# Kernel tuning notes

Hardware: AMD Instinct MI355X
Metric: run time of the kernel (lower is better)

## Reference

```python
import jax, jax.numpy as jnp
import numpy as np

N = 10000
D1, D2, D3, N_INPUT = 20, 256, 128, 500


def setup_inputs() -> dict:
    key = jax.random.key(0)
    k1, k2, k3, k4, k5 = jax.random.split(key, 5)
    z_igae = jax.random.normal(k1, (N, D1), dtype=jnp.float32)
    # row-stochastic-ish dense (normalized) adjacency stand-in
    adj = jax.random.uniform(k2, (N, N), dtype=jnp.float32) / N
    w3 = jax.random.normal(k3, (D1, D2), dtype=jnp.float32) * 0.1
    w4 = jax.random.normal(k4, (D2, D3), dtype=jnp.float32) * 0.1
    w5 = jax.random.normal(k5, (D3, N_INPUT), dtype=jnp.float32) * 0.1
    return {"z_igae": z_igae, "adj": adj, "w3": w3, "w4": w4, "w5": w5}


def reference(z_igae, adj, w3, w4, w5):
    # GNNLayer: spmm(adj, x @ W), tanh activation when active=True
    z = jnp.tanh(adj @ (z_igae @ w3))        # [N, D2]
    z = jnp.tanh(adj @ (z @ w4))             # [N, D3]
    z_hat = adj @ (z @ w5)                   # [N, n_input], active=False
    z_hat_adj = jax.nn.sigmoid(z_hat @ z_hat.T)  # [N, N] dense reconstruction
    return (z_hat, z_hat_adj)
```

## Files before the change

kernel.cpp:

```cpp
#include <hip/hip_runtime.h>
#include <cstddef>
#include <cstdint>


typedef __attribute__((ext_vector_type(8))) short bf16x8;
typedef __attribute__((ext_vector_type(4))) float f32x4;

#define NROWS 10000
#define MP    10048
#define MPAD  10112

__device__ inline unsigned short f2bf(float f) {
  union { float f; unsigned int u; } a; a.f = f;
  unsigned int u = a.u;
  u += 0x7fffu + ((u >> 16) & 1u);
  return (unsigned short)(u >> 16);
}

__device__ inline void gl_lds16(const void* g, void* l) {
  __builtin_amdgcn_global_load_lds(
      (const __attribute__((address_space(1))) void*)g,
      (__attribute__((address_space(3))) void*)l, 16, 0, 0);
}

__global__ __launch_bounds__(256)
void gemm1_fused(const float* __restrict__ adj, const short* __restrict__ zt,
                 short* __restrict__ adjb, float* __restrict__ P,
                 int kChunks, int S) {
  __shared__ short As[64 * 64];
  __shared__ short Bs[32 * 64];
  const int tid  = threadIdx.x;
  const int wave = tid >> 6;
  const int lane = tid & 63;
  const int row0 = blockIdx.y * 64;
  const int s    = blockIdx.z;
  const int t0 = (int)((long long)s * kChunks / S);
  const int t1 = (int)((long long)(s + 1) * kChunks / S);

  f32x4 acc[2];
#pragma unroll
  for (int i = 0; i < 2; ++i) acc[i] = (f32x4){0.f, 0.f, 0.f, 0.f};

  const int lr = lane >> 3;
  const int lk = ((lane & 7) ^ lr) * 8;
  const int fr = lane & 15, fq = lane >> 4, sw = lane & 7;

  const int ar  = tid >> 2;
  const int acq = tid & 3;
  const int gr  = row0 + ar;
  const bool rv = gr < NROWS;

  for (int t = t0; t < t1; ++t) {
    const int k0 = t * 64;
    __syncthreads();
    gl_lds16(zt + (size_t)(8 * wave + lr) * MP + k0 + lk, (void*)(Bs + wave * 512));
    const int gc = k0 + acq * 16;
    float4 f[4];
#pragma unroll
    for (int j = 0; j < 4; ++j) {
      int c = gc + 4 * j;
      f[j] = (rv && c < NROWS) ? *(const float4*)(adj + (size_t)gr * NROWS + c)
                               : make_float4(0.f, 0.f, 0.f, 0.f);
    }
    unsigned short h[16] __attribute__((aligned(16)));
#pragma unroll
    for (int j = 0; j < 4; ++j) {
      h[4 * j + 0] = f2bf(f[j].x); h[4 * j + 1] = f2bf(f[j].y);
      h[4 * j + 2] = f2bf(f[j].z); h[4 * j + 3] = f2bf(f[j].w);
    }
    *(uint4*)(adjb + (size_t)gr * MP + gc)     = *(const uint4*)&h[0];
    *(uint4*)(adjb + (size_t)gr * MP + gc + 8) = *(const uint4*)&h[8];
    *(bf16x8*)&As[ar * 64 + ((acq * 2 + 0) ^ (ar & 7)) * 8] = *(const bf16x8*)&h[0];
    *(bf16x8*)&As[ar * 64 + ((acq * 2 + 1) ^ (ar & 7)) * 8] = *(const bf16x8*)&h[8];
    __syncthreads();
#pragma unroll
    for (int ks = 0; ks < 2; ++ks) {
      const int go = ((ks * 4 + fq) ^ sw) * 8;
      bf16x8 af = *(const bf16x8*)&As[(wave * 16 + fr) * 64 + go];
#pragma unroll
      for (int nt = 0; nt < 2; ++nt) {
        bf16x8 bfr = *(const bf16x8*)&Bs[(nt * 16 + fr) * 64 + go];
        acc[nt] = __builtin_amdgcn_mfma_f32_16x16x32_bf16(af, bfr, acc[nt], 0, 0, 0);
      }
    }
  }
  float* Cs = P + (size_t)s * MPAD * 32;
  const int rbase = row0 + wave * 16 + (lane >> 4) * 4;
  const int cbase = lane & 15;
#pragma unroll
  for (int nt = 0; nt < 2; ++nt) {
    const int cc = cbase + nt * 16;
#pragma unroll
    for (int r = 0; r < 4; ++r)
      Cs[(size_t)(rbase + r) * 32 + cc] = acc[nt][r];
  }
}

__global__ __launch_bounds__(256)
void gemm_adj(const short* __restrict__ A, const short* __restrict__ Bt,
              float* __restrict__ P, int kChunks, int S) {
  __shared__ short As[128 * 64];
  __shared__ short Bs[128 * 64];
  const int tid  = threadIdx.x;
  const int wave = tid >> 6;
  const int lane = tid & 63;
  const int row0 = blockIdx.y * 128;
  const int s    = blockIdx.z;
  const int t0 = (int)((long long)s * kChunks / S);
  const int t1 = (int)((long long)(s + 1) * kChunks / S);
  const int wr = wave >> 1, wc = wave & 1;

  f32x4 acc[4][4];
#pragma unroll
  for (int m = 0; m < 4; ++m)
#pragma unroll
    for (int n = 0; n < 4; ++n) acc[m][n] = (f32x4){0.f, 0.f, 0.f, 0.f};

  const int lr = lane >> 3;
  const int lk = ((lane & 7) ^ lr) * 8;
  const int fr = lane & 15, fq = lane >> 4, sw = lane & 7;

  for (int t = t0; t < t1; ++t) {
    const int k0 = t * 64;
    __syncthreads();
#pragma unroll
    for (int i = 0; i < 4; ++i) {
      int c = wave + 4 * i;
      gl_lds16(A + (size_t)(row0 + 8 * c + lr) * MP + k0 + lk, (void*)(As + c * 512));
      gl_lds16(Bt + (size_t)(8 * c + lr) * MP + k0 + lk, (void*)(Bs + c * 512));
    }
    __syncthreads();
#pragma unroll
    for (int ks = 0; ks < 2; ++ks) {
      const int go = ((ks * 4 + fq) ^ sw) * 8;
      bf16x8 av[4], bv[4];
#pragma unroll
      for (int m = 0; m < 4; ++m)
        av[m] = *(const bf16x8*)&As[(wr * 64 + m * 16 + fr) * 64 + go];
#pragma unroll
      for (int n = 0; n < 4; ++n)
        bv[n] = *(const bf16x8*)&Bs[(wc * 64 + n * 16 + fr) * 64 + go];
#pragma unroll
      for (int m = 0; m < 4; ++m)
#pragma unroll
        for (int n = 0; n < 4; ++n)
          acc[m][n] = __builtin_amdgcn_mfma_f32_16x16x32_bf16(av[m], bv[n], acc[m][n], 0, 0, 0);
    }
  }

  float* Cs = P + (size_t)s * MPAD * 128;
  const int q = lane >> 4;
#pragma unroll
  for (int m = 0; m < 4; ++m) {
    const int rb = row0 + wr * 64 + m * 16 + q * 4;
#pragma unroll
    for (int n = 0; n < 4; ++n) {
      const int cc = wc * 64 + n * 16 + fr;
#pragma unroll
      for (int r = 0; r < 4; ++r)
        Cs[(size_t)(rb + r) * 128 + cc] = acc[m][n][r];
    }
  }
}

__global__ __launch_bounds__(256)
void gemm_recon(const short* __restrict__ A, const short* __restrict__ Bt,
                float* __restrict__ C) {
  __shared__ short As[128 * 64];
  __shared__ short Bs[128 * 64];
  const int tid  = threadIdx.x;
  const int wave = tid >> 6;
  const int lane = tid & 63;
  const int row0 = blockIdx.y * 128;
  const int col0 = blockIdx.x * 128;

  f32x4 acc[2][8];
#pragma unroll
  for (int i = 0; i < 2; ++i)
#pragma unroll
    for (int j = 0; j < 8; ++j) acc[i][j] = (f32x4){0.f, 0.f, 0.f, 0.f};

  const int lr = lane >> 3;
  const int lk = ((lane & 7) ^ lr) * 8;
  const int fr = lane & 15, fq = lane >> 4, sw = lane & 7;

  for (int t = 0; t < 2; ++t) {
    const int k0 = t * 64;
    __syncthreads();
#pragma unroll
    for (int i = 0; i < 4; ++i) {
      int c = wave + 4 * i;
      gl_lds16(A + (size_t)(row0 + 8 * c + lr) * 128 + k0 + lk, (void*)(As + c * 512));
      gl_lds16(Bt + (size_t)(col0 + 8 * c + lr) * 128 + k0 + lk, (void*)(Bs + c * 512));
    }
    __syncthreads();
#pragma unroll
    for (int ks = 0; ks < 2; ++ks) {
      const int go = ((ks * 4 + fq) ^ sw) * 8;
      bf16x8 a0 = *(const bf16x8*)&As[(wave * 32 + fr) * 64 + go];
      bf16x8 a1 = *(const bf16x8*)&As[(wave * 32 + 16 + fr) * 64 + go];
#pragma unroll
      for (int nt = 0; nt < 8; ++nt) {
        bf16x8 bfr = *(const bf16x8*)&Bs[(nt * 16 + fr) * 64 + go];
        acc[0][nt] = __builtin_amdgcn_mfma_f32_16x16x32_bf16(a0, bfr, acc[0][nt], 0, 0, 0);
        acc[1][nt] = __builtin_amdgcn_mfma_f32_16x16x32_bf16(a1, bfr, acc[1][nt], 0, 0, 0);
      }
    }
  }

  const int q = lane >> 4;
#pragma unroll
  for (int mf = 0; mf < 2; ++mf) {
    const int rb = row0 + wave * 32 + mf * 16 + q * 4;
#pragma unroll
    for (int nt = 0; nt < 8; ++nt) {
      const int cc = col0 + nt * 16 + (lane & 15);
      if (cc >= NROWS) continue;
#pragma unroll
      for (int r = 0; r < 4; ++r) {
        const int rr = rb + r;
        if (rr < NROWS) {
          float v = acc[mf][nt][r];
          v = 1.0f / (1.0f + __expf(-v));
          C[(size_t)rr * NROWS + cc] = v;
        }
      }
    }
  }
}

__global__ __launch_bounds__(256)
void midchain(const float* __restrict__ P, const float* __restrict__ w3,
              const float* __restrict__ w4, short* __restrict__ t2t) {
  __shared__ float w3s[20][256];
  __shared__ float g1s[64][36];
  __shared__ float z1s[64][260];
  __shared__ float bufB[64][132];
  const int tid = threadIdx.x;
  const int m0  = blockIdx.x * 64;

  for (int j = tid; j < 20 * 256; j += 256) w3s[j >> 8][j & 255] = w3[j];
  {
    const int r = tid >> 2, c0 = (tid & 3) * 8;
    f32x4 s0 = {0.f, 0.f, 0.f, 0.f}, s1 = {0.f, 0.f, 0.f, 0.f};
#pragma unroll
    for (int i = 0; i < 8; ++i) {
      const float* p = P + (size_t)i * MPAD * 32 + (size_t)(m0 + r) * 32 + c0;
      s0 += *(const f32x4*)p;
      s1 += *(const f32x4*)(p + 4);
    }
    *(f32x4*)&g1s[r][c0] = s0;
    *(f32x4*)&g1s[r][c0 + 4] = s1;
  }
  __syncthreads();
  {
    const int r = tid >> 2, c0 = (tid & 3) * 64;
    float a[20];
#pragma unroll
    for (int k = 0; k < 20; ++k) a[k] = g1s[r][k];
    for (int c = 0; c < 64; c += 4) {
      f32x4 s = {0.f, 0.f, 0.f, 0.f};
#pragma unroll
      for (int k = 0; k < 20; ++k) s += a[k] * *(const f32x4*)&w3s[k][c0 + c];
      z1s[r][c0 + c + 0] = tanhf(s[0]); z1s[r][c0 + c + 1] = tanhf(s[1]);
      z1s[r][c0 + c + 2] = tanhf(s[2]); z1s[r][c0 + c + 3] = tanhf(s[3]);
    }
  }
  const int r = tid >> 2, c0 = (tid & 3) * 32;
  float acc[32];
#pragma unroll
  for (int j = 0; j < 32; ++j) acc[j] = 0.f;
  for (int kt = 0; kt < 4; ++kt) {
    __syncthreads();
    {
      const int lr = tid >> 2, lc = (tid & 3) * 32;
#pragma unroll
      for (int j = 0; j < 32; j += 4)
        *(f32x4*)&bufB[lr][lc + j] =
            *(const f32x4*)(w4 + (size_t)(kt * 64 + lr) * 128 + lc + j);
    }
    __syncthreads();
    for (int k = 0; k < 64; ++k) {
      const float a = z1s[r][kt * 64 + k];
#pragma unroll
      for (int j = 0; j < 32; j += 4) {
        f32x4 w = *(const f32x4*)&bufB[k][c0 + j];
        acc[j + 0] += a * w[0]; acc[j + 1] += a * w[1];
        acc[j + 2] += a * w[2]; acc[j + 3] += a * w[3];
      }
    }
  }
  __syncthreads();
#pragma unroll
  for (int j = 0; j < 32; j += 4) *(f32x4*)&bufB[r][c0 + j] = *(const f32x4*)&acc[j];
  __syncthreads();
  {
    const int n = tid >> 1, seg = (tid & 1) * 32;
    unsigned short h[32] __attribute__((aligned(16)));
#pragma unroll
    for (int i = 0; i < 32; ++i) h[i] = f2bf(bufB[seg + i][n]);
    uint4* dst = (uint4*)(t2t + (size_t)n * MP + m0 + seg);
    dst[0] = *(const uint4*)&h[0];  dst[1] = *(const uint4*)&h[8];
    dst[2] = *(const uint4*)&h[16]; dst[3] = *(const uint4*)&h[24];
  }
}

__global__ __launch_bounds__(256)
void reduce128h(const float* __restrict__ P, const float* __restrict__ Mm,
                float* __restrict__ g3, short* __restrict__ g3b,
                short* __restrict__ hb) {
  __shared__ float MmS[128 * 128];
  __shared__ float g3t[64][132];
  const int tid = threadIdx.x;
  const int m0  = blockIdx.x * 64;

  for (int j = tid; j < 128 * 128; j += 256) MmS[j] = Mm[j];
  const int r = tid >> 2, c0 = (tid & 3) * 32;
  {
    const int gr = m0 + r;
    for (int c = 0; c < 32; c += 4) {
      f32x4 s = {0.f, 0.f, 0.f, 0.f};
#pragma unroll
      for (int i = 0; i < 8; ++i)
        s += *(const f32x4*)(P + (size_t)i * MPAD * 128 + (size_t)gr * 128 + c0 + c);
      *(f32x4*)&g3t[r][c0 + c] = s;
      *(f32x4*)(g3 + (size_t)gr * 128 + c0 + c) = s;
      short4 sb;
      sb.x = (short)f2bf(s[0]); sb.y = (short)f2bf(s[1]);
      sb.z = (short)f2bf(s[2]); sb.w = (short)f2bf(s[3]);
      *(short4*)(g3b + (size_t)gr * 128 + c0 + c) = sb;
    }
  }
  __syncthreads();
  float acc[32];
#pragma unroll
  for (int j = 0; j < 32; ++j) acc[j] = 0.f;
  for (int k = 0; k < 128; ++k) {
    const float a = g3t[r][k];
#pragma unroll
    for (int j = 0; j < 32; j += 4) {
      const float* mv = &MmS[k * 128 + c0 + j];
      acc[j + 0] += a * mv[0]; acc[j + 1] += a * mv[1];
      acc[j + 2] += a * mv[2]; acc[j + 3] += a * mv[3];
    }
  }
  unsigned short h[32] __attribute__((aligned(16)));
#pragma unroll
  for (int j = 0; j < 32; ++j) h[j] = f2bf(acc[j]);
  uint4* dst = (uint4*)(hb + (size_t)(m0 + r) * 128 + c0);
  dst[0] = *(const uint4*)&h[0]; dst[1] = *(const uint4*)&h[8];
  dst[2] = *(const uint4*)&h[16]; dst[3] = *(const uint4*)&h[24];
}

#define TK 16
#define TM 64
#define TN 64

template <int ACT>
__global__ __launch_bounds__(256)
void gemm_nn_f32(const float* __restrict__ A, int lda,
                 const float* __restrict__ B, int ldb,
                 float* __restrict__ C, int ldc, int M, int N, int K) {
  __shared__ float Asm[TK][TM + 4];
  __shared__ float Bsm[TK][TN + 4];
  const int tid = threadIdx.x;
  const int tx = tid & 15, ty = tid >> 4;
  const int row0 = blockIdx.y * TM, col0 = blockIdx.x * TN;
  const int a_m = tid >> 2, a_k = (tid & 3) << 2;
  const int b_k = tid >> 4, b_n = (tid & 15) << 2;
  float acc[4][4] = {};
  const int ntile = (K + TK - 1) / TK;

  auto ld_a = [&](int k0) {
    float4 v = make_float4(0.f, 0.f, 0.f, 0.f);
    int r = row0 + a_m, k = k0 + a_k;
    if (r < M && k < K) v = *(const float4*)(A + (size_t)r * lda + k);
    return v;
  };
  auto ld_b = [&](int k0) {
    float4 v = make_float4(0.f, 0.f, 0.f, 0.f);
    int k = k0 + b_k, c = col0 + b_n;
    if (k < K && c + 3 < N) v = *(const float4*)(B + (size_t)k * ldb + c);
    return v;
  };

  float4 pa = ld_a(0), pb = ld_b(0);
  for (int t = 0; t < ntile; ++t) {
    __syncthreads();
    Asm[a_k + 0][a_m] = pa.x; Asm[a_k + 1][a_m] = pa.y;
    Asm[a_k + 2][a_m] = pa.z; Asm[a_k + 3][a_m] = pa.w;
    *(float4*)&Bsm[b_k][b_n] = pb;
    __syncthreads();
    if (t + 1 < ntile) { pa = ld_a((t + 1) * TK); pb = ld_b((t + 1) * TK); }
#pragma unroll
    for (int kk = 0; kk < TK; ++kk) {
      float4 a = *(const float4*)&Asm[kk][ty << 2];
      float4 b = *(const float4*)&Bsm[kk][tx << 2];
      float av[4] = {a.x, a.y, a.z, a.w};
      float bv[4] = {b.x, b.y, b.z, b.w};
#pragma unroll
      for (int i = 0; i < 4; ++i)
#pragma unroll
        for (int j = 0; j < 4; ++j) acc[i][j] += av[i] * bv[j];
    }
  }
#pragma unroll
  for (int i = 0; i < 4; ++i) {
    int r = row0 + (ty << 2) + i;
    if (r >= M) continue;
#pragma unroll
    for (int j = 0; j < 4; ++j) {
      int c = col0 + (tx << 2) + j;
      if (c >= N) continue;
      float v = acc[i][j];
      if (ACT == 1) v = tanhf(v);
      C[(size_t)r * ldc + c] = v;
    }
  }
}

__global__ __launch_bounds__(256)
void gemm_nt_f32(const float* __restrict__ A, int lda,
                 const float* __restrict__ B, int ldb,
                 float* __restrict__ C, int ldc, int M, int N, int K) {
  __shared__ float Asm[TK][TM + 4];
  __shared__ float Bsm[TK][TN + 4];
  const int tid = threadIdx.x;
  const int tx = tid & 15, ty = tid >> 4;
  const int row0 = blockIdx.y * TM, col0 = blockIdx.x * TN;
  const int a_m = tid >> 2, a_k = (tid & 3) << 2;
  const int b_n = tid >> 2, b_k = (tid & 3) << 2;
  float acc[4][4] = {};
  const int ntile = (K + TK - 1) / TK;

  auto ld_a = [&](int k0) {
    float4 v = make_float4(0.f, 0.f, 0.f, 0.f);
    int r = row0 + a_m, k = k0 + a_k;
    if (r < M && k + 3 < K) v = *(const float4*)(A + (size_t)r * lda + k);
    return v;
  };
  auto ld_b = [&](int k0) {
    float4 v = make_float4(0.f, 0.f, 0.f, 0.f);
    int c = col0 + b_n, k = k0 + b_k;
    if (c < N && k + 3 < K) v = *(const float4*)(B + (size_t)c * ldb + k);
    return v;
  };

  float4 pa = ld_a(0), pb = ld_b(0);
  for (int t = 0; t < ntile; ++t) {
    __syncthreads();
    Asm[a_k + 0][a_m] = pa.x; Asm[a_k + 1][a_m] = pa.y;
    Asm[a_k + 2][a_m] = pa.z; Asm[a_k + 3][a_m] = pa.w;
    Bsm[b_k + 0][b_n] = pb.x; Bsm[b_k + 1][b_n] = pb.y;
    Bsm[b_k + 2][b_n] = pb.z; Bsm[b_k + 3][b_n] = pb.w;
    __syncthreads();
    if (t + 1 < ntile) { pa = ld_a((t + 1) * TK); pb = ld_b((t + 1) * TK); }
#pragma unroll
    for (int kk = 0; kk < TK; ++kk) {
      float4 a = *(const float4*)&Asm[kk][ty << 2];
      float4 b = *(const float4*)&Bsm[kk][tx << 2];
      float av[4] = {a.x, a.y, a.z, a.w};
      float bv[4] = {b.x, b.y, b.z, b.w};
#pragma unroll
      for (int i = 0; i < 4; ++i)
#pragma unroll
        for (int j = 0; j < 4; ++j) acc[i][j] += av[i] * bv[j];
    }
  }
#pragma unroll
  for (int i = 0; i < 4; ++i) {
    int r = row0 + (ty << 2) + i;
    if (r >= M) continue;
#pragma unroll
    for (int j = 0; j < 4; ++j) {
      int c = col0 + (tx << 2) + j;
      if (c >= N) continue;
      C[(size_t)r * ldc + c] = acc[i][j];
    }
  }
}


__global__ void tr_zigae(const float* __restrict__ z, short* __restrict__ zt) {
  int m = blockIdx.x * 256 + threadIdx.x;
  int n = blockIdx.y;
  if (m >= MP) return;
  float v = (n < 20 && m < NROWS) ? z[(size_t)m * 20 + n] : 0.f;
  zt[(size_t)n * MP + m] = f2bf(v);
}

__global__ __launch_bounds__(256)
void reduce_tr(const float* __restrict__ P, short* __restrict__ z2t) {
  __shared__ float T[128][33];
  const int tid = threadIdx.x;
  const int m0 = blockIdx.x * 32;
  const int mr = tid >> 5;
  const int n0 = (tid & 31) * 4;
#pragma unroll
  for (int g = 0; g < 4; ++g) {
    const int mm = g * 8 + mr;
    const int m = m0 + mm;
    f32x4 sAcc = (f32x4){0.f, 0.f, 0.f, 0.f};
#pragma unroll
    for (int i = 0; i < 8; ++i)
      sAcc += *(const f32x4*)(P + (size_t)i * MPAD * 128 + (size_t)m * 128 + n0);
    if (m < NROWS) {
      T[n0 + 0][mm] = tanhf(sAcc[0]); T[n0 + 1][mm] = tanhf(sAcc[1]);
      T[n0 + 2][mm] = tanhf(sAcc[2]); T[n0 + 3][mm] = tanhf(sAcc[3]);
    } else {
      T[n0 + 0][mm] = 0.f; T[n0 + 1][mm] = 0.f;
      T[n0 + 2][mm] = 0.f; T[n0 + 3][mm] = 0.f;
    }
  }
  __syncthreads();
  const int n = tid >> 1, mh = (tid & 1) * 16;
  unsigned short h[16] __attribute__((aligned(16)));
#pragma unroll
  for (int j = 0; j < 16; ++j) h[j] = f2bf(T[n][mh + j]);
  *(uint4*)(z2t + (size_t)n * MP + m0 + mh)     = *(const uint4*)&h[0];
  *(uint4*)(z2t + (size_t)n * MP + m0 + mh + 8) = *(const uint4*)&h[8];
}

extern "C" void kernel_launch(void* const* d_in, const int* in_sizes, int n_in,
                              void* d_out, int out_size, void* d_ws, size_t ws_size,
                              hipStream_t stream) {
  const float* z_igae = (const float*)d_in[0];
  const float* adj    = (const float*)d_in[1];
  const float* w3     = (const float*)d_in[2];
  const float* w4     = (const float*)d_in[3];
  const float* w5     = (const float*)d_in[4];

  const int M = NROWS, D2 = 256, D3 = 128, NI = 500;
  const int S = 8, KC = MP / 64;

  float* z_hat   = (float*)d_out;
  float* out_adj = (float*)d_out + (size_t)M * NI;

  char* oa = (char*)out_adj;
  short* adjb = (short*)oa;
  float* P    = (float*)(oa + 204ll * 1024 * 1024);
  char*  sc   = oa + 248ll * 1024 * 1024;
  short* t2t  = (short*)(sc);
  short* z2t  = (short*)(sc + 3ll * 1024 * 1024);
  short* zt   = (short*)(sc + 6ll * 1024 * 1024);
  float* Mm   = (float*)(sc + 7ll * 1024 * 1024);
  float* g3   = (float*)(sc + 8ll * 1024 * 1024);

  short* hb  = (short*)d_ws;
  short* g3b = (short*)d_ws + (size_t)MPAD * 128;

  dim3 blk(256);

  gemm_nt_f32<<<dim3(2, 2), blk, 0, stream>>>(w5, NI, w5, NI, Mm, D3, D3, D3, NI);
  tr_zigae<<<dim3(40, 32), blk, 0, stream>>>(z_igae, zt);
  gemm1_fused<<<dim3(1, 158, S), blk, 0, stream>>>(adj, zt, adjb, P, KC, S);
  midchain<<<dim3(157), blk, 0, stream>>>(P, w3, w4, t2t);
  gemm_adj<<<dim3(1, 79, S), blk, 0, stream>>>(adjb, t2t, P, KC, S);
  reduce_tr<<<dim3(314), blk, 0, stream>>>(P, z2t);
  gemm_adj<<<dim3(1, 79, S), blk, 0, stream>>>(adjb, z2t, P, KC, S);
  reduce128h<<<dim3(158), blk, 0, stream>>>(P, Mm, g3, g3b, hb);
  gemm_nn_f32<0><<<dim3(8, 157), blk, 0, stream>>>(g3, D3, w5, NI, z_hat, NI, M, NI, D3);
  gemm_recon<<<dim3(79, 79), blk, 0, stream>>>(hb, g3b, out_adj);
}
```

Measured before the change: 1.084 ms.

## Raise first GEMM split-K, remap recon tiles per XCD, preload both K halves

The first adjacency GEMM now uses 16 split-K slices instead of 8, so more workgroups cover the long K dimension; the midchain reduction sums 16 partials to match. The reconstruction GEMM remaps workgroup IDs so that contiguous tiles land on the same XCD for L2 reuse, loads both 64-wide K halves into double LDS buffers behind a single barrier, and raises wave priority around the MFMA loop. This costs more LDS and more partial-sum traffic through P in exchange for more parallelism and fewer barriers.

```diff
diff --git a/kernel.cpp b/kernel.cpp
--- a/kernel.cpp
+++ b/kernel.cpp
@@ -9,6 +9,8 @@
 #define NROWS 10000
 #define MP    10048
 #define MPAD  10112
+#define S1    16
+#define S2    8
 
 __device__ inline unsigned short f2bf(float f) {
   union { float f; unsigned int u; } a; a.f = f;
@@ -166,13 +168,17 @@
 __global__ __launch_bounds__(256)
 void gemm_recon(const short* __restrict__ A, const short* __restrict__ Bt,
                 float* __restrict__ C) {
-  __shared__ short As[128 * 64];
-  __shared__ short Bs[128 * 64];
+  __shared__ short As[2][128 * 64];
+  __shared__ short Bs[2][128 * 64];
   const int tid  = threadIdx.x;
   const int wave = tid >> 6;
   const int lane = tid & 63;
-  const int row0 = blockIdx.y * 128;
-  const int col0 = blockIdx.x * 128;
+
+  const int orig = blockIdx.y * 79 + blockIdx.x;
+  const int xcd = orig & 7, idx = orig >> 3;
+  const int wgid = (xcd < 1) ? idx : (781 + (xcd - 1) * 780 + idx);
+  const int row0 = (wgid / 79) * 128;
+  const int col0 = (wgid % 79) * 128;
 
   f32x4 acc[2][8];
 #pragma unroll
@@ -184,27 +190,33 @@
   const int lk = ((lane & 7) ^ lr) * 8;
   const int fr = lane & 15, fq = lane >> 4, sw = lane & 7;
 
+#pragma unroll
   for (int t = 0; t < 2; ++t) {
     const int k0 = t * 64;
-    __syncthreads();
 #pragma unroll
     for (int i = 0; i < 4; ++i) {
       int c = wave + 4 * i;
-      gl_lds16(A + (size_t)(row0 + 8 * c + lr) * 128 + k0 + lk, (void*)(As + c * 512));
-      gl_lds16(Bt + (size_t)(col0 + 8 * c + lr) * 128 + k0 + lk, (void*)(Bs + c * 512));
-    }
-    __syncthreads();
+      gl_lds16(A + (size_t)(row0 + 8 * c + lr) * 128 + k0 + lk, (void*)(&As[t][c * 512]));
+      gl_lds16(Bt + (size_t)(col0 + 8 * c + lr) * 128 + k0 + lk, (void*)(&Bs[t][c * 512]));
+    }
+  }
+  __syncthreads();
+
+#pragma unroll
+  for (int t = 0; t < 2; ++t) {
 #pragma unroll
     for (int ks = 0; ks < 2; ++ks) {
       const int go = ((ks * 4 + fq) ^ sw) * 8;
-      bf16x8 a0 = *(const bf16x8*)&As[(wave * 32 + fr) * 64 + go];
-      bf16x8 a1 = *(const bf16x8*)&As[(wave * 32 + 16 + fr) * 64 + go];
+      bf16x8 a0 = *(const bf16x8*)&As[t][(wave * 32 + fr) * 64 + go];
+      bf16x8 a1 = *(const bf16x8*)&As[t][(wave * 32 + 16 + fr) * 64 + go];
+      __builtin_amdgcn_s_setprio(1);
 #pragma unroll
       for (int nt = 0; nt < 8; ++nt) {
-        bf16x8 bfr = *(const bf16x8*)&Bs[(nt * 16 + fr) * 64 + go];
+        bf16x8 bfr = *(const bf16x8*)&Bs[t][(nt * 16 + fr) * 64 + go];
         acc[0][nt] = __builtin_amdgcn_mfma_f32_16x16x32_bf16(a0, bfr, acc[0][nt], 0, 0, 0);
         acc[1][nt] = __builtin_amdgcn_mfma_f32_16x16x32_bf16(a1, bfr, acc[1][nt], 0, 0, 0);
       }
+      __builtin_amdgcn_s_setprio(0);
     }
   }
 
@@ -244,7 +256,7 @@
     const int r = tid >> 2, c0 = (tid & 3) * 8;
     f32x4 s0 = {0.f, 0.f, 0.f, 0.f}, s1 = {0.f, 0.f, 0.f, 0.f};
 #pragma unroll
-    for (int i = 0; i < 8; ++i) {
+    for (int i = 0; i < S1; ++i) {
       const float* p = P + (size_t)i * MPAD * 32 + (size_t)(m0 + r) * 32 + c0;
       s0 += *(const f32x4*)p;
       s1 += *(const f32x4*)(p + 4);
@@ -321,7 +333,7 @@
     for (int c = 0; c < 32; c += 4) {
       f32x4 s = {0.f, 0.f, 0.f, 0.f};
 #pragma unroll
-      for (int i = 0; i < 8; ++i)
+      for (int i = 0; i < S2; ++i)
         s += *(const f32x4*)(P + (size_t)i * MPAD * 128 + (size_t)gr * 128 + c0 + c);
       *(f32x4*)&g3t[r][c0 + c] = s;
       *(f32x4*)(g3 + (size_t)gr * 128 + c0 + c) = s;
@@ -502,7 +514,7 @@
     const int m = m0 + mm;
     f32x4 sAcc = (f32x4){0.f, 0.f, 0.f, 0.f};
 #pragma unroll
-    for (int i = 0; i < 8; ++i)
+    for (int i = 0; i < S2; ++i)
       sAcc += *(const f32x4*)(P + (size_t)i * MPAD * 128 + (size_t)m * 128 + n0);
     if (m < NROWS) {
       T[n0 + 0][mm] = tanhf(sAcc[0]); T[n0 + 1][mm] = tanhf(sAcc[1]);
@@ -531,7 +543,7 @@
   const float* w5     = (const float*)d_in[4];
 
   const int M = NROWS, D2 = 256, D3 = 128, NI = 500;
-  const int S = 8, KC = MP / 64;
+  const int KC = MP / 64;
 
   float* z_hat   = (float*)d_out;
   float* out_adj = (float*)d_out + (size_t)M * NI;
@@ -553,11 +565,11 @@
 
   gemm_nt_f32<<<dim3(2, 2), blk, 0, stream>>>(w5, NI, w5, NI, Mm, D3, D3, D3, NI);
   tr_zigae<<<dim3(40, 32), blk, 0, stream>>>(z_igae, zt);
-  gemm1_fused<<<dim3(1, 158, S), blk, 0, stream>>>(adj, zt, adjb, P, KC, S);
+  gemm1_fused<<<dim3(1, 158, S1), blk, 0, stream>>>(adj, zt, adjb, P, KC, S1);
   midchain<<<dim3(157), blk, 0, stream>>>(P, w3, w4, t2t);
-  gemm_adj<<<dim3(1, 79, S), blk, 0, stream>>>(adjb, t2t, P, KC, S);
+  gemm_adj<<<dim3(1, 79, S2), blk, 0, stream>>>(adjb, t2t, P, KC, S2);
   reduce_tr<<<dim3(314), blk, 0, stream>>>(P, z2t);
-  gemm_adj<<<dim3(1, 79, S), blk, 0, stream>>>(adjb, z2t, P, KC, S);
+  gemm_adj<<<dim3(1, 79, S2), blk, 0, stream>>>(adjb, z2t, P, KC, S2);
   reduce128h<<<dim3(158), blk, 0, stream>>>(P, Mm, g3, g3b, hb);
   gemm_nn_f32<0><<<dim3(8, 157), blk, 0, stream>>>(g3, D3, w5, NI, z_hat, NI, M, NI, D3);
   gemm_recon<<<dim3(79, 79), blk, 0, stream>>>(hb, g3b, out_adj);
```

After: 1.094 ms. Within noise of the previous version (+0.9%).
